# Optimization experiments

Measured on AMD Instinct MI355X. Metric: run time of the kernel, lower is better.

Reference implementation:

```python
import jax, jax.numpy as jnp
import numpy as np

N = 200000      # total points
B = 4           # number of point clouds
C_IN = 128
C_OUT = 256
GRID = 0.05
EPS = 1e-5      # BatchNorm eps


def setup_inputs() -> dict:
    key = jax.random.key(0)
    ks = jax.random.split(key, 9)
    xyz = jax.random.uniform(ks[0], (1, N, 3), dtype=jnp.float32)
    features = jax.random.normal(ks[1], (1, N, C_IN), dtype=jnp.float32)
    offset = jnp.array([50000, 100000, 150000, 200000], dtype=jnp.int32)
    W1 = jax.random.normal(ks[2], (C_OUT, C_IN), dtype=jnp.float32) * 0.02
    b1 = jax.random.normal(ks[3], (C_OUT,), dtype=jnp.float32) * 0.01
    gamma = jax.random.uniform(ks[4], (C_OUT,), dtype=jnp.float32, minval=0.5, maxval=1.5)
    beta = jax.random.normal(ks[5], (C_OUT,), dtype=jnp.float32) * 0.1
    W2 = jax.random.normal(ks[6], (C_OUT, C_OUT), dtype=jnp.float32) * 0.02
    b2 = jax.random.normal(ks[7], (C_OUT,), dtype=jnp.float32) * 0.01
    return {"xyz": xyz, "features": features, "offset": offset,
            "W1": W1, "b1": b1, "gamma": gamma, "beta": beta, "W2": W2, "b2": b2}


def _offset2batch(offset, n):
    counts = jnp.diff(jnp.concatenate([jnp.zeros((1,), offset.dtype), offset]))
    return jnp.repeat(jnp.arange(offset.shape[0], dtype=jnp.int32), counts,
                      total_repeat_length=n)


def reference(xyz, features, offset, W1, b1, gamma, beta, W2, b2):
    pos = xyz[0]          # [N, 3]
    x = features[0]       # [N, C_IN]
    batch = _offset2batch(offset, pos.shape[0])  # [N]

    # fc: 1x1 conv == linear; BatchNorm1d in training mode (batch stats, biased var)
    h = x @ W1.T + b1                                   # [N, C_OUT]
    mu = h.mean(axis=0)
    var = h.var(axis=0)
    h = (h - mu) / jnp.sqrt(var + EPS) * gamma + beta
    h = jax.nn.relu(h)
    feats = h @ W2.T + b2                               # [N, C_OUT]

    # per-batch min corner (start)
    start = jax.ops.segment_min(pos, batch, num_segments=B)   # [B, 3]

    # voxel grid clustering
    coords = jnp.floor((pos - start[batch]) / GRID).astype(jnp.int32)  # [N, 3] >= 0
    dims = coords.max(axis=0) + 1
    lin = ((batch * dims[0] + coords[:, 0]) * dims[1] + coords[:, 1]) * dims[2] + coords[:, 2]

    uniq, inv, counts = jnp.unique(lin, return_inverse=True, return_counts=True)
    M = uniq.shape[0]

    # segment_csr mean / max over voxels (order-independent, equals sorted CSR reduce)
    xyz_out = jax.ops.segment_sum(pos, inv, num_segments=M) / counts[:, None].astype(pos.dtype)
    feat_out = jax.ops.segment_max(feats, inv, num_segments=M)

    seg_batch = jax.ops.segment_max(batch, inv, num_segments=M)
    offset_out = jnp.cumsum(jnp.bincount(seg_batch, length=B)).astype(offset.dtype)

    return (xyz_out[None], feat_out[None], offset_out, inv)
```

## Files before the change

### kernel.cpp

```cpp
#include <hip/hip_runtime.h>
#include <stdint.h>

#define GRID_SZ 0.05f
#define BN_EPS 1e-5f
#define FLAG_MAGIC 0x7FECA110

typedef __attribute__((ext_vector_type(8))) short bf16x8;
typedef __attribute__((ext_vector_type(4))) float f32x4;

#define WS_START   0
#define WS_DIMS    96
#define WS_CHSUM   128
#define WS_CHSQ    1152
#define WS_AC      2176
#define WS_BC      3200
#define WS_W1B     4224
#define WS_W2B     69760
#define WS_GRAM    200832
#define WS_CSUM    266368
#define WS_HIST    266880
#define WS_RANK    529024
#define WS_CURS    791296
#define WS_BSUM    1053440
#define WS_XYZS    1053952
#define WS_LIN     1840384
#define WS_PERM    2640384
#define WS_XB      3440384

__device__ __forceinline__ short f2bf(float f) {
  unsigned u = __float_as_uint(f);
  u += 0x7FFFu + ((u >> 16) & 1u);
  return (short)(u >> 16);
}

__device__ __forceinline__ bf16x8 load_frag(const float* p) {
  f32x4 a = *(const f32x4*)p;
  f32x4 b = *(const f32x4*)(p + 4);
  bf16x8 r;
  r[0] = f2bf(a[0]); r[1] = f2bf(a[1]); r[2] = f2bf(a[2]); r[3] = f2bf(a[3]);
  r[4] = f2bf(b[0]); r[5] = f2bf(b[1]); r[6] = f2bf(b[2]); r[7] = f2bf(b[3]);
  return r;
}

__device__ __forceinline__ int batch_of(int p, const int* offs, int nb) {
  int b = 0;
  while (b < nb - 1 && p >= offs[b]) b++;
  return b;
}

__device__ __forceinline__ float dec16(unsigned e) {
  unsigned us = (e & 0x8000u) ? (e & 0x7FFFu) : (~e & 0xFFFFu);
  return __uint_as_float(us << 16);
}

__device__ __forceinline__ void dims_of(const unsigned* gstart, int nb,
                                        int& m0, int& m1, int& m2) {
  m0 = 0; m1 = 0; m2 = 0;
  for (int b = 0; b < nb; b++) {
    float s0 = __uint_as_float(gstart[b * 3 + 0]);
    float s1 = __uint_as_float(gstart[b * 3 + 1]);
    float s2 = __uint_as_float(gstart[b * 3 + 2]);
    float x0 = __uint_as_float(gstart[12 + b * 3 + 0]);
    float x1 = __uint_as_float(gstart[12 + b * 3 + 1]);
    float x2 = __uint_as_float(gstart[12 + b * 3 + 2]);
    m0 = max(m0, (int)floorf((x0 - s0) / GRID_SZ));
    m1 = max(m1, (int)floorf((x1 - s1) / GRID_SZ));
    m2 = max(m2, (int)floorf((x2 - s2) / GRID_SZ));
  }
}

__global__ void k_init(unsigned* featU, size_t featN, int* hist, float* xyzs,
                       float* chsum, float* chsq, float* gram, float* csum,
                       unsigned* gstart,
                       const float* __restrict__ W1, const float* __restrict__ W2,
                       short* __restrict__ W1b, short* __restrict__ W2b) {
  size_t i = (size_t)blockIdx.x * blockDim.x + threadIdx.x;
  size_t stride = (size_t)gridDim.x * blockDim.x;
  if (i < 4096) *(bf16x8*)(W1b + i * 8) = load_frag(W1 + i * 8);
  else if (i < 12288) { size_t j = i - 4096; *(bf16x8*)(W2b + j * 8) = load_frag(W2 + j * 8); }
  for (size_t j = i; j < featN; j += stride) featU[j] = 0u;
  for (size_t j = i; j < 65536; j += stride) hist[j] = 0;
  for (size_t j = i; j < 65536u * 3; j += stride) xyzs[j] = 0.f;
  for (size_t j = i; j < 16384; j += stride) gram[j] = 0.f;
  if (i < 256) { chsum[i] = 0.f; chsq[i] = 0.f; }
  if (i < 128) csum[i] = 0.f;
  if (i < 12) gstart[i] = 0x7F800000u;
  else if (i < 24) gstart[i] = 0u;
}

__global__ void k_min(const float* __restrict__ pos, const int* __restrict__ offs,
                      int N, int nb, unsigned* gstart) {
  __shared__ unsigned smin[12], smax[12];
  int tid = threadIdx.x;
  if (tid < 12) { smin[tid] = 0x7F800000u; smax[tid] = 0u; }
  __syncthreads();
  int p = blockIdx.x * blockDim.x + tid;
  if (p < N) {
    int b = batch_of(p, offs, nb);
    for (int c = 0; c < 3; c++) {
      unsigned u = __float_as_uint(pos[p * 3 + c]);
      atomicMin(&smin[b * 3 + c], u);
      atomicMax(&smax[b * 3 + c], u);
    }
  }
  __syncthreads();
  if (tid < 3 * nb) {
    atomicMin(&gstart[tid], smin[tid]);
    atomicMax(&gstart[12 + tid], smax[tid]);
  }
}

__global__ void k_hist(const float* __restrict__ pos, const int* __restrict__ offs,
                       int N, int nb, const unsigned* gstart,
                       int* lin, int* hist, float* xyzs, int* gdims) {
  int m0, m1, m2;
  dims_of(gstart, nb, m0, m1, m2);
  int p = blockIdx.x * blockDim.x + threadIdx.x;
  if (blockIdx.x == 0 && threadIdx.x == 0) { gdims[0] = m0; gdims[1] = m1; gdims[2] = m2; }
  if (p >= N) return;
  int b = batch_of(p, offs, nb);
  int d0 = m0 + 1, d1 = m1 + 1, d2 = m2 + 1;
  int c[3];
  for (int i = 0; i < 3; i++) {
    float s = __uint_as_float(gstart[b * 3 + i]);
    c[i] = (int)floorf((pos[p * 3 + i] - s) / GRID_SZ);
  }
  int li = ((b * d0 + c[0]) * d1 + c[1]) * d2 + c[2];
  if (li < 0 || li >= 65536) li = 0;
  lin[p] = li;
  atomicAdd(&hist[li], 1);
  atomicAdd(&xyzs[li * 3 + 0], pos[p * 3 + 0]);
  atomicAdd(&xyzs[li * 3 + 1], pos[p * 3 + 1]);
  atomicAdd(&xyzs[li * 3 + 2], pos[p * 3 + 2]);
}

__global__ __launch_bounds__(1024) void k_scanA(const int* __restrict__ hist,
                                                const int* __restrict__ gdims, int nb,
                                                int2* bsum) {
  __shared__ int so[16], sc2[16];
  int d0 = gdims[0] + 1, d1 = gdims[1] + 1, d2 = gdims[2] + 1;
  int bins = nb * d0 * d1 * d2;
  if (bins > 65536) bins = 65536;
  int i = blockIdx.x * 1024 + threadIdx.x;
  int o = 0, c = 0;
  if (i < bins) { int h = hist[i]; o = (h > 0); c = h; }
  for (int d = 1; d < 64; d <<= 1) { o += __shfl_xor(o, d); c += __shfl_xor(c, d); }
  int w = threadIdx.x >> 6;
  if ((threadIdx.x & 63) == 0) { so[w] = o; sc2[w] = c; }
  __syncthreads();
  if (threadIdx.x == 0) {
    int O = 0, C = 0;
    for (int k = 0; k < 16; k++) { O += so[k]; C += sc2[k]; }
    bsum[blockIdx.x] = make_int2(O, C);
  }
}

__global__ __launch_bounds__(1024) void k_scanB(const int* __restrict__ hist,
                                                const int* __restrict__ gdims, int nb,
                                                const int2* __restrict__ bsum,
                                                int* rank, int* cursor) {
  __shared__ int so[1024], sc2[1024];
  __shared__ int sbase[2];
  int d0 = gdims[0] + 1, d1 = gdims[1] + 1, d2 = gdims[2] + 1;
  int bins = nb * d0 * d1 * d2;
  if (bins > 65536) bins = 65536;
  int b = blockIdx.x;
  int tid = threadIdx.x;
  if (tid == 0) {
    int O = 0, C = 0;
    for (int k = 0; k < b; k++) { int2 s = bsum[k]; O += s.x; C += s.y; }
    sbase[0] = O; sbase[1] = C;
  }
  int i = b * 1024 + tid;
  int h = (i < bins) ? hist[i] : 0;
  int o = (h > 0), c = h;
  so[tid] = o; sc2[tid] = c;
  __syncthreads();
  for (int off = 1; off < 1024; off <<= 1) {
    int vo = (tid >= off) ? so[tid - off] : 0;
    int vc = (tid >= off) ? sc2[tid - off] : 0;
    __syncthreads();
    so[tid] += vo; sc2[tid] += vc;
    __syncthreads();
  }
  if (i < bins) {
    rank[i]   = sbase[0] + so[tid] - o;
    cursor[i] = sbase[1] + sc2[tid] - c;
  }
  if (i == bins - 1) rank[bins] = sbase[0] + so[tid];
}

template <bool XBF>
__global__ void k_scatter(const int* __restrict__ lin, const int* __restrict__ rank,
                          int* cursor, int N, const float* __restrict__ X,
                          short* __restrict__ Xb, int* __restrict__ permvox,
                          float* __restrict__ out_inv) {
  int p = blockIdx.x * blockDim.x + threadIdx.x;
  if (p >= N) return;
  int li = lin[p];
  int r = rank[li];
  out_inv[p] = (float)r;
  int slot = atomicAdd(&cursor[li], 1);
  if (XBF) {
    permvox[slot] = r;
    const float* src = X + (size_t)p * 128;
    short* dst = Xb + (size_t)slot * 128;
#pragma unroll
    for (int j = 0; j < 16; j++)
      *(bf16x8*)(dst + j * 8) = load_frag(src + j * 8);
  } else {
    permvox[slot] = p;
  }
}

__global__ void k_voxfin(const int* __restrict__ hist, const int* __restrict__ rank,
                         const float* __restrict__ xyzs, const int* __restrict__ gdims,
                         int nb, float* out_xyz, float* out_off) {
  int d0 = gdims[0] + 1, d1 = gdims[1] + 1, d2 = gdims[2] + 1;
  int dxyz = d0 * d1 * d2;
  int bins = nb * dxyz;
  if (bins > 65536) bins = 65536;
  int i = blockIdx.x * blockDim.x + threadIdx.x;
  if (blockIdx.x == 0 && (int)threadIdx.x < nb) {
    int t = (int)threadIdx.x;
    int idx = (t + 1) * dxyz; if (idx > bins) idx = bins;
    out_off[t] = (float)rank[idx];
  }
  if (i >= bins) return;
  int cnt = hist[i];
  if (cnt <= 0) return;
  int v = rank[i];
  float fc = (float)cnt;
  out_xyz[v * 3 + 0] = xyzs[i * 3 + 0] / fc;
  out_xyz[v * 3 + 1] = xyzs[i * 3 + 1] / fc;
  out_xyz[v * 3 + 2] = xyzs[i * 3 + 2] / fc;
}

#define GCHUNK 1024
__global__ __launch_bounds__(256, 2) void k_gram(const short* __restrict__ Xb, int N,
                                                 float* __restrict__ gram,
                                                 float* __restrict__ csum) {
  __shared__ short xt[128 * 72];
  __shared__ float lcs[128];
  int tid = threadIdx.x;
  int wid = tid >> 6, lane = tid & 63;
  int lr = lane & 15, lg = lane >> 4;
  int base = blockIdx.x * GCHUNK;
  int cg = tid & 7;
  float cs[16];
#pragma unroll
  for (int j = 0; j < 16; j++) cs[j] = 0.f;
  f32x4 acc[2][8];
#pragma unroll
  for (int a = 0; a < 2; a++)
#pragma unroll
    for (int b = 0; b < 8; b++) acc[a][b] = (f32x4){0.f, 0.f, 0.f, 0.f};

  for (int k0 = 0; k0 < GCHUNK; k0 += 64) {
    __syncthreads();
#pragma unroll
    for (int it = 0; it < 2; it++) {
      int task = tid + it * 256;
      int r = task >> 3;
      int row = base + k0 + r;
      bf16x8 v0 = {0,0,0,0,0,0,0,0}, v1 = {0,0,0,0,0,0,0,0};
      if (row < N) {
        const short* src = Xb + (size_t)row * 128 + cg * 16;
        v0 = *(const bf16x8*)src;
        v1 = *(const bf16x8*)(src + 8);
      }
#pragma unroll
      for (int j = 0; j < 8; j++) {
        cs[j]     += __uint_as_float(((unsigned)(unsigned short)v0[j]) << 16);
        cs[j + 8] += __uint_as_float(((unsigned)(unsigned short)v1[j]) << 16);
      }
      int rs = r ^ (cg << 3);
#pragma unroll
      for (int j = 0; j < 8; j++) {
        xt[(cg * 16 + j) * 72 + rs]     = v0[j];
        xt[(cg * 16 + 8 + j) * 72 + rs] = v1[j];
      }
    }
    __syncthreads();
#pragma unroll
    for (int ks = 0; ks < 2; ks++) {
      int kk = ks * 32 + lg * 8;
      bf16x8 f[8], af[2];
#pragma unroll
      for (int s = 0; s < 8; s++)
        f[s] = *(const bf16x8*)(xt + (s * 16 + lr) * 72 + (kk ^ (s << 3)));
#pragma unroll
      for (int a = 0; a < 2; a++) {
        int ti = wid * 2 + a;
        af[a] = *(const bf16x8*)(xt + (ti * 16 + lr) * 72 + (kk ^ (ti << 3)));
      }
#pragma unroll
      for (int a = 0; a < 2; a++)
#pragma unroll
        for (int b = 0; b < 8; b++)
          acc[a][b] = __builtin_amdgcn_mfma_f32_16x16x32_bf16(af[a], f[b], acc[a][b], 0, 0, 0);
    }
  }
#pragma unroll
  for (int a = 0; a < 2; a++)
#pragma unroll
    for (int b = 0; b < 8; b++)
#pragma unroll
      for (int r_ = 0; r_ < 4; r_++) {
        int ci = (wid * 2 + a) * 16 + lg * 4 + r_;
        int cj = b * 16 + lr;
        atomicAdd(&gram[ci * 128 + cj], acc[a][b][r_]);
      }
  if (tid < 128) lcs[tid] = 0.f;
  __syncthreads();
#pragma unroll
  for (int j = 0; j < 16; j++) atomicAdd(&lcs[cg * 16 + j], cs[j]);
  __syncthreads();
  if (tid < 128) atomicAdd(&csum[tid], lcs[tid]);
}

__global__ __launch_bounds__(128) void k_finalizeG(const float* __restrict__ gram,
                                                   const float* __restrict__ csum,
                                                   const float* __restrict__ W1,
                                                   const float* __restrict__ b1,
                                                   const float* __restrict__ gamma,
                                                   const float* __restrict__ beta,
                                                   int N, float* Ac, float* Bc) {
  __shared__ float w[128], red[128], red2[128];
  int c = blockIdx.x, j = threadIdx.x;
  w[j] = W1[c * 128 + j];
  __syncthreads();
  float t = 0.f;
  for (int k = 0; k < 128; k++) t += gram[k * 128 + j] * w[k];
  red[j]  = t * w[j];
  red2[j] = w[j] * csum[j];
  __syncthreads();
  for (int off = 64; off > 0; off >>= 1) {
    if (j < off) { red[j] += red[j + off]; red2[j] += red2[j + off]; }
    __syncthreads();
  }
  if (j == 0) {
    float fn = (float)N;
    float q  = red[0] / fn;
    float md = red2[0] / fn;
    float b  = b1[c];
    float mu = md + b;
    float e2 = q + 2.f * b * md + b * b;
    float var = e2 - mu * mu;
    float s = gamma[c] * rsqrtf(var + BN_EPS);
    Ac[c] = s;
    Bc[c] = (b - mu) * s + beta[c];
  }
}

__global__ __launch_bounds__(256) void k_statsA(const float* __restrict__ X,
                                                const short* __restrict__ W1b,
                                                const float* __restrict__ b1, int N,
                                                float* chsum, float* chsq) {
  int tid = threadIdx.x;
  int wid = tid >> 6, lane = tid & 63;
  int lr = lane & 15, lg = lane >> 4;
  int p0 = blockIdx.x * 64;
  int wcol = wid * 64;
  f32x4 acc[4][4] = {};
  for (int kk = 0; kk < 4; kk++) {
    int k = kk * 32 + lg * 8;
    bf16x8 af[4], bfr[4];
    for (int m = 0; m < 4; m++) {
      int row = p0 + m * 16 + lr; if (row >= N) row = N - 1;
      af[m] = load_frag(X + (size_t)row * 128 + k);
    }
    for (int n = 0; n < 4; n++)
      bfr[n] = *(const bf16x8*)(W1b + (size_t)(wcol + n * 16 + lr) * 128 + k);
    for (int m = 0; m < 4; m++)
      for (int n = 0; n < 4; n++)
        acc[m][n] = __builtin_amdgcn_mfma_f32_16x16x32_bf16(af[m], bfr[n], acc[m][n], 0, 0, 0);
  }
  for (int n = 0; n < 4; n++) {
    int c = wcol + n * 16 + lr;
    float bv = b1[c];
    float s1 = 0.f, s2 = 0.f;
    for (int m = 0; m < 4; m++)
      for (int r = 0; r < 4; r++) {
        int row = p0 + m * 16 + lg * 4 + r;
        if (row < N) {
          float h = acc[m][n][r] + bv;
          s1 += h; s2 += h * h;
        }
      }
    s1 += __shfl_xor(s1, 16); s2 += __shfl_xor(s2, 16);
    s1 += __shfl_xor(s1, 32); s2 += __shfl_xor(s2, 32);
    if (lg == 0) { atomicAdd(&chsum[c], s1); atomicAdd(&chsq[c], s2); }
  }
}

__global__ void k_finalize(const float* chsum, const float* chsq, const float* b1,
                           const float* gamma, const float* beta, int N,
                           float* Ac, float* Bc) {
  int c = threadIdx.x;
  float fn = (float)N;
  float mu = chsum[c] / fn;
  float var = chsq[c] / fn - mu * mu;
  float s = gamma[c] * rsqrtf(var + BN_EPS);
  Ac[c] = s;
  Bc[c] = (b1[c] - mu) * s + beta[c];
}

template <bool XBF>
__global__ __launch_bounds__(256, 3) void k_gemmB(const float* __restrict__ X,
                                                  const short* __restrict__ Xb,
                                                  const short* __restrict__ W1b,
                                                  const short* __restrict__ W2b,
                                                  const float* __restrict__ b2,
                                                  const float* __restrict__ Ac,
                                                  const float* __restrict__ Bc,
                                                  const int* __restrict__ permvox,
                                                  const int* __restrict__ lin,
                                                  const int* __restrict__ rank,
                                                  int N, unsigned* __restrict__ featU,
                                                  int* __restrict__ bflag) {
  __shared__ char smem[64 * 264 * 2];
  __shared__ int vox_s[64];
  __shared__ int perm_s[64];
  char* axt  = smem;
  char* ylds = smem;
  unsigned short* lmax = (unsigned short*)smem;

  int tid = threadIdx.x;
  int wid = tid >> 6, lane = tid & 63;
  int lr = lane & 15, lg = lane >> 4;
  int p0 = blockIdx.x * 64;
  int wcol = wid * 64;

  if (tid < 64) {
    int s = p0 + tid;
    if (XBF) {
      vox_s[tid] = (s < N) ? permvox[s] : -1;
    } else {
      int pp = permvox[(s < N) ? s : (N - 1)];
      perm_s[tid] = pp;
      vox_s[tid] = (s < N) ? rank[lin[pp]] : -1;
    }
  }
  __syncthreads();

  {
    int row = tid >> 2, chunk = tid & 3;
    int base = row * 256 + chunk * 64;
    int sw = (row & 7) << 4;
    bf16x8 a0, a1, a2, a3;
    if (XBF) {
      int grow = p0 + row; if (grow >= N) grow = N - 1;
      const short* src = Xb + (size_t)grow * 128 + chunk * 32;
      a0 = *(const bf16x8*)(src);
      a1 = *(const bf16x8*)(src + 8);
      a2 = *(const bf16x8*)(src + 16);
      a3 = *(const bf16x8*)(src + 24);
    } else {
      int prow = perm_s[row];
      const float* src = X + (size_t)prow * 128 + chunk * 32;
      a0 = load_frag(src);
      a1 = load_frag(src + 8);
      a2 = load_frag(src + 16);
      a3 = load_frag(src + 24);
    }
    *(bf16x8*)(axt + ((base)      ^ sw)) = a0;
    *(bf16x8*)(axt + ((base + 16) ^ sw)) = a1;
    *(bf16x8*)(axt + ((base + 32) ^ sw)) = a2;
    *(bf16x8*)(axt + ((base + 48) ^ sw)) = a3;
  }
  __syncthreads();

  f32x4 acc[4][4] = {};
  for (int kk = 0; kk < 4; kk++) {
    int kbyte = kk * 64 + lg * 16;
    bf16x8 af[4], bfr[4];
    int sw = (lr & 7) << 4;
    for (int m = 0; m < 4; m++) {
      int rowA = m * 16 + lr;
      af[m] = *(const bf16x8*)(axt + ((rowA * 256 + kbyte) ^ sw));
    }
    int k = kk * 32 + lg * 8;
    for (int n = 0; n < 4; n++)
      bfr[n] = *(const bf16x8*)(W1b + (size_t)(wcol + n * 16 + lr) * 128 + k);
    for (int m = 0; m < 4; m++)
      for (int n = 0; n < 4; n++)
        acc[m][n] = __builtin_amdgcn_mfma_f32_16x16x32_bf16(af[m], bfr[n], acc[m][n], 0, 0, 0);
  }
  __syncthreads();

  for (int n = 0; n < 4; n++) {
    int c = wcol + n * 16 + lr;
    float Av = Ac[c], Bv = Bc[c];
    int colb = c * 2;
    for (int m = 0; m < 4; m++)
      for (int r = 0; r < 4; r++) {
        int row = m * 16 + lg * 4 + r;
        float y = fmaxf(acc[m][n][r] * Av + Bv, 0.0f);
        int addr = (row * 512 + colb) ^ ((row & 7) << 4);
        *(short*)(ylds + addr) = f2bf(y);
      }
  }
  __syncthreads();

  f32x4 acc2[4][4] = {};
  for (int kk = 0; kk < 8; kk++) {
    int k = kk * 32 + lg * 8;
    int kb = k * 2;
    bf16x8 af[4], bfr[4];
    for (int m = 0; m < 4; m++) {
      int row = m * 16 + lr;
      af[m] = *(const bf16x8*)(ylds + ((row * 512 + kb) ^ ((row & 7) << 4)));
    }
    for (int n = 0; n < 4; n++)
      bfr[n] = *(const bf16x8*)(W2b + (size_t)(wcol + n * 16 + lr) * 256 + k);
    for (int m = 0; m < 4; m++)
      for (int n = 0; n < 4; n++)
        acc2[m][n] = __builtin_amdgcn_mfma_f32_16x16x32_bf16(af[m], bfr[n], acc2[m][n], 0, 0, 0);
  }
  __syncthreads();

  for (int n = 0; n < 4; n++) {
    int c = wcol + n * 16 + lr;
    float bv = b2[c];
    for (int m = 0; m < 4; m++)
      for (int r = 0; r < 4; r++) {
        int row = m * 16 + lg * 4 + r;
        unsigned us = (unsigned)(unsigned short)f2bf(acc2[m][n][r] + bv);
        us = (us & 0x8000u) ? (~us & 0xFFFFu) : (us | 0x8000u);
        lmax[row * 264 + c] = (unsigned short)us;
      }
  }
  __syncthreads();

  int nrows = N - p0; if (nrows > 64) nrows = 64;
  int c = tid;
  unsigned run = 0;
  int vprev = vox_s[0];
  int run_start = 0;
  for (int row = 0; row < nrows; row++) {
    int v = vox_s[row];
    if (v != vprev) {
      size_t idx = (size_t)vprev * 256 + c;
      if (run_start > 0) {
        ((float*)featU)[idx] = dec16(run);
      } else {
        atomicMax(&featU[idx], run << 16);
        if (tid == 0) bflag[vprev] = FLAG_MAGIC;
      }
      run = 0; vprev = v; run_start = row;
    }
    run = max(run, (unsigned)lmax[row * 264 + c]);
  }
  atomicMax(&featU[(size_t)vprev * 256 + c], run << 16);
  if (tid == 0) bflag[vprev] = FLAG_MAGIC;
}

__global__ void k_decode(unsigned* featU, const int* __restrict__ bflag, size_t n) {
  size_t i = (size_t)blockIdx.x * blockDim.x + threadIdx.x;
  size_t stride = (size_t)gridDim.x * blockDim.x;
  for (; i < n; i += stride) {
    if (bflag[i >> 8] == FLAG_MAGIC) {
      unsigned e = featU[i] >> 16;
      ((float*)featU)[i] = dec16(e);
    }
  }
}

extern "C" void kernel_launch(void* const* d_in, const int* in_sizes, int n_in,
                              void* d_out, int out_size, void* d_ws, size_t ws_size,
                              hipStream_t stream) {
  const float* xyz   = (const float*)d_in[0];
  const float* X     = (const float*)d_in[1];
  const int*   offs  = (const int*)d_in[2];
  const float* W1    = (const float*)d_in[3];
  const float* b1    = (const float*)d_in[4];
  const float* gamma = (const float*)d_in[5];
  const float* beta  = (const float*)d_in[6];
  const float* W2    = (const float*)d_in[7];
  const float* b2    = (const float*)d_in[8];

  int N  = in_sizes[0] / 3;
  int nb = in_sizes[2];
  int M  = (out_size - nb - N) / 259;
  if (M <= 0) return;

  char* ws = (char*)d_ws;
  unsigned* gstart = (unsigned*)(ws + WS_START);
  int*   gdims  = (int*)(ws + WS_DIMS);
  float* chsum  = (float*)(ws + WS_CHSUM);
  float* chsq   = (float*)(ws + WS_CHSQ);
  float* Ac     = (float*)(ws + WS_AC);
  float* Bc     = (float*)(ws + WS_BC);
  short* W1b    = (short*)(ws + WS_W1B);
  short* W2b    = (short*)(ws + WS_W2B);
  float* gram   = (float*)(ws + WS_GRAM);
  float* csum   = (float*)(ws + WS_CSUM);
  int*   hist   = (int*)(ws + WS_HIST);
  int*   rank   = (int*)(ws + WS_RANK);
  int*   cursor = (int*)(ws + WS_CURS);
  int2*  bsum   = (int2*)(ws + WS_BSUM);
  float* xyzs   = (float*)(ws + WS_XYZS);
  int*   lin    = (int*)(ws + WS_LIN);
  int*   permvox = (int*)(ws + WS_PERM);
  short* Xb     = (short*)(ws + WS_XB);

  size_t req = (size_t)WS_XB + (size_t)N * 128 * 2;
  bool xbf = ws_size >= req;

  float* out_xyz  = (float*)d_out;
  float* out_feat = out_xyz + (size_t)3 * M;
  float* out_off  = out_feat + (size_t)M * 256;
  float* out_inv  = out_off + nb;
  unsigned* featU = (unsigned*)out_feat;

  int npb = (N + 255) / 256;
  int ngb = (N + 63) / 64;
  int ngr = (N + GCHUNK - 1) / GCHUNK;

  hipLaunchKernelGGL(k_init, dim3(2048), dim3(256), 0, stream,
                     featU, (size_t)M * 256, hist, xyzs, chsum, chsq, gram, csum,
                     gstart, W1, W2, W1b, W2b);
  hipLaunchKernelGGL(k_min, dim3(npb), dim3(256), 0, stream, xyz, offs, N, nb, gstart);
  hipLaunchKernelGGL(k_hist, dim3(npb), dim3(256), 0, stream,
                     xyz, offs, N, nb, gstart, lin, hist, xyzs, gdims);
  hipLaunchKernelGGL(k_scanA, dim3(64), dim3(1024), 0, stream, hist, gdims, nb, bsum);
  hipLaunchKernelGGL(k_scanB, dim3(64), dim3(1024), 0, stream,
                     hist, gdims, nb, bsum, rank, cursor);
  hipLaunchKernelGGL(k_voxfin, dim3(256), dim3(256), 0, stream,
                     hist, rank, xyzs, gdims, nb, out_xyz, out_off);
  if (xbf) {
    hipLaunchKernelGGL((k_scatter<true>), dim3(npb), dim3(256), 0, stream,
                       lin, rank, cursor, N, X, Xb, permvox, out_inv);
    hipLaunchKernelGGL(k_gram, dim3(ngr), dim3(256), 0, stream, Xb, N, gram, csum);
    hipLaunchKernelGGL(k_finalizeG, dim3(256), dim3(128), 0, stream,
                       gram, csum, W1, b1, gamma, beta, N, Ac, Bc);
    hipLaunchKernelGGL((k_gemmB<true>), dim3(ngb), dim3(256), 0, stream,
                       X, Xb, W1b, W2b, b2, Ac, Bc, permvox, lin, rank, N, featU, cursor);
  } else {
    hipLaunchKernelGGL((k_scatter<false>), dim3(npb), dim3(256), 0, stream,
                       lin, rank, cursor, N, X, Xb, permvox, out_inv);
    hipLaunchKernelGGL(k_statsA, dim3(ngb), dim3(256), 0, stream,
                       X, W1b, b1, N, chsum, chsq);
    hipLaunchKernelGGL(k_finalize, dim3(1), dim3(256), 0, stream,
                       chsum, chsq, b1, gamma, beta, N, Ac, Bc);
    hipLaunchKernelGGL((k_gemmB<false>), dim3(ngb), dim3(256), 0, stream,
                       X, Xb, W1b, W2b, b2, Ac, Bc, permvox, lin, rank, N, featU, cursor);
  }
  hipLaunchKernelGGL(k_decode, dim3(2048), dim3(256), 0, stream,
                     featU, cursor, (size_t)M * 256);
}
```

Baseline: 298.3 us.

## Fuse voxel finalize into scan, double-buffer gram tiles, zero only boundary voxels

Folds the voxel centroid and offset output into the second scan kernel, which removes one launch. The full memset of the feature output is replaced by a small kernel that zeroes only the voxel rows touched by atomics at 64-row tile boundaries, since interior runs are written directly. The Gram kernel now double-buffers its LDS tile, prefetching the next 64 rows while MFMAs run on the current one. Each offset thread loops over the batches, and correctness depends on every non-boundary voxel row being fully overwritten.

Result: no change. 293.3 us (-1.7%).

```diff
diff --git a/kernel.cpp b/kernel.cpp
--- a/kernel.cpp
+++ b/kernel.cpp
@@ -158,7 +158,10 @@
 __global__ __launch_bounds__(1024) void k_scanB(const int* __restrict__ hist,
                                                 const int* __restrict__ gdims, int nb,
                                                 const int2* __restrict__ bsum,
-                                                int* rank, int* cursor) {
+                                                int* rank, int* cursor,
+                                                const float* __restrict__ xyzs,
+                                                float* __restrict__ out_xyz,
+                                                float* __restrict__ out_off) {
   __shared__ int so[1024], sc2[1024];
   __shared__ int sbase[2];
   int d0 = gdims[0] + 1, d1 = gdims[1] + 1, d2 = gdims[2] + 1;
@@ -184,8 +187,21 @@
     __syncthreads();
   }
   if (i < bins) {
-    rank[i]   = sbase[0] + so[tid] - o;
+    int rk = sbase[0] + so[tid] - o;
+    rank[i]   = rk;
     cursor[i] = sbase[1] + sc2[tid] - c;
+    if (h > 0) {
+      float fc = (float)h;
+      out_xyz[rk * 3 + 0] = xyzs[i * 3 + 0] / fc;
+      out_xyz[rk * 3 + 1] = xyzs[i * 3 + 1] / fc;
+      out_xyz[rk * 3 + 2] = xyzs[i * 3 + 2] / fc;
+    }
+    int dxyz = d0 * d1 * d2;
+    for (int t = 0; t < nb; t++) {
+      int idx = (t + 1) * dxyz; if (idx > bins) idx = bins;
+      if (idx < bins) { if (i == idx) out_off[t] = (float)rk; }
+      else if (i == bins - 1) out_off[t] = (float)(sbase[0] + so[tid]);
+    }
   }
   if (i == bins - 1) rank[bins] = sbase[0] + so[tid];
 }
@@ -213,40 +229,31 @@
   }
 }
 
-__global__ void k_voxfin(const int* __restrict__ hist, const int* __restrict__ rank,
-                         const float* __restrict__ xyzs, const int* __restrict__ gdims,
-                         int nb, float* out_xyz, float* out_off) {
-  int d0 = gdims[0] + 1, d1 = gdims[1] + 1, d2 = gdims[2] + 1;
-  int dxyz = d0 * d1 * d2;
-  int bins = nb * dxyz;
-  if (bins > 65536) bins = 65536;
-  int i = blockIdx.x * blockDim.x + threadIdx.x;
-  if (blockIdx.x == 0 && (int)threadIdx.x < nb) {
-    int t = (int)threadIdx.x;
-    int idx = (t + 1) * dxyz; if (idx > bins) idx = bins;
-    out_off[t] = (float)rank[idx];
-  }
-  if (i >= bins) return;
-  int cnt = hist[i];
-  if (cnt <= 0) return;
-  int v = rank[i];
-  float fc = (float)cnt;
-  out_xyz[v * 3 + 0] = xyzs[i * 3 + 0] / fc;
-  out_xyz[v * 3 + 1] = xyzs[i * 3 + 1] / fc;
-  out_xyz[v * 3 + 2] = xyzs[i * 3 + 2] / fc;
+__global__ void k_initb(const int* __restrict__ permvox, int N,
+                        unsigned* __restrict__ featU) {
+  int inst = blockIdx.x;
+  int k = inst >> 1;
+  int s = k * 64 + ((inst & 1) ? 63 : 0);
+  if (s >= N) s = N - 1;
+  int v = permvox[s];
+  featU[(size_t)v * 256 + threadIdx.x] = 0u;
 }
 
 #define GCHUNK 1024
+#define XTSZ (128 * 72)
 __global__ __launch_bounds__(256, 2) void k_gram(const short* __restrict__ Xb, int N,
                                                  float* __restrict__ gram,
                                                  float* __restrict__ csum) {
-  __shared__ short xt[128 * 72];
+  __shared__ short xt[2 * XTSZ];
   __shared__ float lcs[128];
   int tid = threadIdx.x;
   int wid = tid >> 6, lane = tid & 63;
   int lr = lane & 15, lg = lane >> 4;
   int base = blockIdx.x * GCHUNK;
   int cg = tid & 7;
+  int r0 = tid >> 3;
+  int r1 = (tid + 256) >> 3;
+  int rsA = r0 ^ (cg << 3), rsB = r1 ^ (cg << 3);
   float cs[16];
 #pragma unroll
   for (int j = 0; j < 16; j++) cs[j] = 0.f;
@@ -256,49 +263,85 @@
 #pragma unroll
     for (int b = 0; b < 8; b++) acc[a][b] = (f32x4){0.f, 0.f, 0.f, 0.f};
 
-  for (int k0 = 0; k0 < GCHUNK; k0 += 64) {
+  {
+    bf16x8 a0 = {0,0,0,0,0,0,0,0}, a1 = a0, b0 = a0, b1 = a0;
+    int rowA = base + r0, rowB = base + r1;
+    if (rowA < N) {
+      const short* s = Xb + (size_t)rowA * 128 + cg * 16;
+      a0 = *(const bf16x8*)s; a1 = *(const bf16x8*)(s + 8);
+    }
+    if (rowB < N) {
+      const short* s = Xb + (size_t)rowB * 128 + cg * 16;
+      b0 = *(const bf16x8*)s; b1 = *(const bf16x8*)(s + 8);
+    }
+#pragma unroll
+    for (int j = 0; j < 8; j++) {
+      cs[j]     += __uint_as_float(((unsigned)(unsigned short)a0[j]) << 16)
+                 + __uint_as_float(((unsigned)(unsigned short)b0[j]) << 16);
+      cs[j + 8] += __uint_as_float(((unsigned)(unsigned short)a1[j]) << 16)
+                 + __uint_as_float(((unsigned)(unsigned short)b1[j]) << 16);
+    }
+#pragma unroll
+    for (int j = 0; j < 8; j++) {
+      xt[(cg * 16 + j) * 72 + rsA]     = a0[j];
+      xt[(cg * 16 + 8 + j) * 72 + rsA] = a1[j];
+      xt[(cg * 16 + j) * 72 + rsB]     = b0[j];
+      xt[(cg * 16 + 8 + j) * 72 + rsB] = b1[j];
+    }
+  }
+
+  int nst = GCHUNK / 64;
+  for (int st = 0; st < nst; st++) {
+    short* cur = xt + (st & 1) * XTSZ;
+    short* nxt = xt + ((st & 1) ^ 1) * XTSZ;
     __syncthreads();
-#pragma unroll
-    for (int it = 0; it < 2; it++) {
-      int task = tid + it * 256;
-      int r = task >> 3;
-      int row = base + k0 + r;
-      bf16x8 v0 = {0,0,0,0,0,0,0,0}, v1 = {0,0,0,0,0,0,0,0};
-      if (row < N) {
-        const short* src = Xb + (size_t)row * 128 + cg * 16;
-        v0 = *(const bf16x8*)src;
-        v1 = *(const bf16x8*)(src + 8);
-      }
-#pragma unroll
-      for (int j = 0; j < 8; j++) {
-        cs[j]     += __uint_as_float(((unsigned)(unsigned short)v0[j]) << 16);
-        cs[j + 8] += __uint_as_float(((unsigned)(unsigned short)v1[j]) << 16);
-      }
-      int rs = r ^ (cg << 3);
-#pragma unroll
-      for (int j = 0; j < 8; j++) {
-        xt[(cg * 16 + j) * 72 + rs]     = v0[j];
-        xt[(cg * 16 + 8 + j) * 72 + rs] = v1[j];
-      }
-    }
-    __syncthreads();
+    bf16x8 a0 = {0,0,0,0,0,0,0,0}, a1 = a0, b0 = a0, b1 = a0;
+    bool hn = (st + 1 < nst);
+    if (hn) {
+      int rowA = base + (st + 1) * 64 + r0;
+      int rowB = base + (st + 1) * 64 + r1;
+      if (rowA < N) {
+        const short* s = Xb + (size_t)rowA * 128 + cg * 16;
+        a0 = *(const bf16x8*)s; a1 = *(const bf16x8*)(s + 8);
+      }
+      if (rowB < N) {
+        const short* s = Xb + (size_t)rowB * 128 + cg * 16;
+        b0 = *(const bf16x8*)s; b1 = *(const bf16x8*)(s + 8);
+      }
+    }
 #pragma unroll
     for (int ks = 0; ks < 2; ks++) {
       int kk = ks * 32 + lg * 8;
       bf16x8 f[8], af[2];
 #pragma unroll
       for (int s = 0; s < 8; s++)
-        f[s] = *(const bf16x8*)(xt + (s * 16 + lr) * 72 + (kk ^ (s << 3)));
+        f[s] = *(const bf16x8*)(cur + (s * 16 + lr) * 72 + (kk ^ (s << 3)));
 #pragma unroll
       for (int a = 0; a < 2; a++) {
         int ti = wid * 2 + a;
-        af[a] = *(const bf16x8*)(xt + (ti * 16 + lr) * 72 + (kk ^ (ti << 3)));
+        af[a] = *(const bf16x8*)(cur + (ti * 16 + lr) * 72 + (kk ^ (ti << 3)));
       }
 #pragma unroll
       for (int a = 0; a < 2; a++)
 #pragma unroll
         for (int b = 0; b < 8; b++)
           acc[a][b] = __builtin_amdgcn_mfma_f32_16x16x32_bf16(af[a], f[b], acc[a][b], 0, 0, 0);
+    }
+    if (hn) {
+#pragma unroll
+      for (int j = 0; j < 8; j++) {
+        cs[j]     += __uint_as_float(((unsigned)(unsigned short)a0[j]) << 16)
+                   + __uint_as_float(((unsigned)(unsigned short)b0[j]) << 16);
+        cs[j + 8] += __uint_as_float(((unsigned)(unsigned short)a1[j]) << 16)
+                   + __uint_as_float(((unsigned)(unsigned short)b1[j]) << 16);
+      }
+#pragma unroll
+      for (int j = 0; j < 8; j++) {
+        nxt[(cg * 16 + j) * 72 + rsA]     = a0[j];
+        nxt[(cg * 16 + 8 + j) * 72 + rsA] = a1[j];
+        nxt[(cg * 16 + j) * 72 + rsB]     = b0[j];
+        nxt[(cg * 16 + 8 + j) * 72 + rsB] = b1[j];
+      }
     }
   }
 #pragma unroll
@@ -552,8 +595,10 @@
     }
     run = max(run, (unsigned)lmax[row * 264 + c]);
   }
-  atomicMax(&featU[(size_t)vprev * 256 + c], run << 16);
-  if (tid == 0) bflag[vprev] = FLAG_MAGIC;
+  if (vprev >= 0) {
+    atomicMax(&featU[(size_t)vprev * 256 + c], run << 16);
+    if (tid == 0) bflag[vprev] = FLAG_MAGIC;
+  }
 }
 
 __global__ void k_decode(unsigned* featU, const int* __restrict__ bflag, size_t n) {
@@ -619,19 +664,19 @@
   int ngr = (N + GCHUNK - 1) / GCHUNK;
 
   hipLaunchKernelGGL(k_init, dim3(2048), dim3(256), 0, stream,
-                     featU, (size_t)M * 256, hist, xyzs, chsum, chsq, gram, csum,
-                     gstart, W1, W2, W1b, W2b);
+                     featU, xbf ? (size_t)0 : (size_t)M * 256, hist, xyzs,
+                     chsum, chsq, gram, csum, gstart, W1, W2, W1b, W2b);
   hipLaunchKernelGGL(k_min, dim3(npb), dim3(256), 0, stream, xyz, offs, N, nb, gstart);
   hipLaunchKernelGGL(k_hist, dim3(npb), dim3(256), 0, stream,
                      xyz, offs, N, nb, gstart, lin, hist, xyzs, gdims);
   hipLaunchKernelGGL(k_scanA, dim3(64), dim3(1024), 0, stream, hist, gdims, nb, bsum);
   hipLaunchKernelGGL(k_scanB, dim3(64), dim3(1024), 0, stream,
-                     hist, gdims, nb, bsum, rank, cursor);
-  hipLaunchKernelGGL(k_voxfin, dim3(256), dim3(256), 0, stream,
-                     hist, rank, xyzs, gdims, nb, out_xyz, out_off);
+                     hist, gdims, nb, bsum, rank, cursor, xyzs, out_xyz, out_off);
   if (xbf) {
     hipLaunchKernelGGL((k_scatter<true>), dim3(npb), dim3(256), 0, stream,
                        lin, rank, cursor, N, X, Xb, permvox, out_inv);
+    hipLaunchKernelGGL(k_initb, dim3(2 * ngb), dim3(256), 0, stream,
+                       permvox, N, featU);
     hipLaunchKernelGGL(k_gram, dim3(ngr), dim3(256), 0, stream, Xb, N, gram, csum);
     hipLaunchKernelGGL(k_finalizeG, dim3(256), dim3(128), 0, stream,
                        gram, csum, W1, b1, gamma, beta, N, Ac, Bc);
```
